# Kernel optimization log

Measured on AMD Instinct MI355X. Metric: run time of the kernel, lower is better.

## Reference

```python
import jax, jax.numpy as jnp
import numpy as np

TEXT_VOCAB = 32000
NUM_CODEBOOKS = 8
CODEBOOK_SIZE = 1024
SLICE = CODEBOOK_SIZE + 2  # codebook slice length incl. BOS/EOS
AUDIO_VOCAB = NUM_CODEBOOKS * SLICE  # 8208
HIDDEN = 2048
NH = 16
NKV = 8
HD = HIDDEN // NH  # 128
FFN = 8192
LAYERS = 2
EPS = 1e-5


def setup_inputs() -> dict:
    key = jax.random.key(0)
    ks = jax.random.split(key, 16)
    s = 0.02
    qkv_dim = (NH + 2 * NKV) * HD  # 4096
    inp = {
        "input_ids": jax.random.randint(ks[0], (2, 1024), 0, TEXT_VOCAB + CODEBOOK_SIZE, dtype=jnp.int32),
        "vocab_embed": jax.random.normal(ks[1], (TEXT_VOCAB, HIDDEN), jnp.float32) * s,
        "audio_embed": jax.random.normal(ks[2], (AUDIO_VOCAB, HIDDEN), jnp.float32) * s,
        "ln_in": jnp.ones((LAYERS, HIDDEN), jnp.float32),
        "ln_audio_in": jnp.ones((LAYERS, HIDDEN), jnp.float32),
        "ln_post": jnp.ones((LAYERS, HIDDEN), jnp.float32),
        "ln_audio_post": jnp.ones((LAYERS, HIDDEN), jnp.float32),
        "w_qkv": jax.random.normal(ks[3], (LAYERS, HIDDEN, qkv_dim), jnp.float32) * s,
        "w_o": jax.random.normal(ks[4], (LAYERS, NH * HD, HIDDEN), jnp.float32) * s,
        "w_fc": jax.random.normal(ks[5], (LAYERS, HIDDEN, FFN), jnp.float32) * s,
        "w_proj": jax.random.normal(ks[6], (LAYERS, FFN, HIDDEN), jnp.float32) * s,
        "w_audio_fc": jax.random.normal(ks[7], (LAYERS, HIDDEN, FFN), jnp.float32) * s,
        "w_audio_proj": jax.random.normal(ks[8], (LAYERS, FFN, HIDDEN), jnp.float32) * s,
        "ln_f": jnp.ones((HIDDEN,), jnp.float32),
    }
    return inp


def _rms(x, w):
    return x * jax.lax.rsqrt(jnp.mean(x * x, axis=-1, keepdims=True) + EPS) * w


def reference(input_ids, vocab_embed, audio_embed, ln_in, ln_audio_in, ln_post,
              ln_audio_post, w_qkv, w_o, w_fc, w_proj, w_audio_fc, w_audio_proj, ln_f):
    B, S = input_ids.shape
    audio_mask = input_ids > TEXT_VOCAB - 1  # [B,S] bool
    mask3 = audio_mask[..., None]

    # --- embedding ---
    text_ids = jnp.where(audio_mask, TEXT_VOCAB - 1, input_ids)
    text_e = vocab_embed[text_ids]  # [B,S,H]
    audio_ids = jnp.where(audio_mask, input_ids - TEXT_VOCAB, 0)
    shift = jnp.arange(NUM_CODEBOOKS, dtype=jnp.int32) * SLICE  # [C]
    audio_e = audio_embed[audio_ids[None] + shift[:, None, None]].sum(0)  # [B,S,H]
    h = jnp.where(mask3, audio_e, text_e)

    causal = jnp.tril(jnp.ones((S, S), bool))
    scale = 1.0 / np.sqrt(HD)

    def layer(h, p):
        li, lai, lp, lap, wqkv, wo, wfc, wpr, wafc, wapr = p
        # dual-path input norm (both computed, merged by mask)
        x = jnp.where(mask3, _rms(h, lai), _rms(h, li))
        # causal GQA attention
        qkv = x @ wqkv
        q = qkv[..., : NH * HD].reshape(B, S, NH, HD)
        k = qkv[..., NH * HD:(NH + NKV) * HD].reshape(B, S, NKV, HD)
        v = qkv[..., (NH + NKV) * HD:].reshape(B, S, NKV, HD)
        rep = NH // NKV
        k = jnp.repeat(k, rep, axis=2)
        v = jnp.repeat(v, rep, axis=2)
        scores = jnp.einsum('bqhd,bkhd->bhqk', q, k) * scale
        scores = jnp.where(causal, scores, jnp.finfo(scores.dtype).min)
        attn = jax.nn.softmax(scores, axis=-1)
        o = jnp.einsum('bhqk,bkhd->bqhd', attn, v).reshape(B, S, NH * HD) @ wo
        h = h + o
        # dual-path FFN (both computed, merged by mask)
        y_text = jax.nn.silu(_rms(h, lp) @ wfc) @ wpr
        y_audio = jax.nn.silu(_rms(h, lap) @ wafc) @ wapr
        h = h + jnp.where(mask3, y_audio, y_text)
        return h, None

    params = (ln_in, ln_audio_in, ln_post, ln_audio_post,
              w_qkv, w_o, w_fc, w_proj, w_audio_fc, w_audio_proj)
    h, _ = jax.lax.scan(layer, h, params)
    return _rms(h, ln_f)
```

## Files before the change

kernel.cpp:

```cpp
#include <hip/hip_runtime.h>
#include <hip/hip_bf16.h>

typedef unsigned short u16;
typedef __attribute__((ext_vector_type(4))) float f32x4;
typedef __attribute__((ext_vector_type(8))) short bf16x8;
typedef __attribute__((ext_vector_type(8))) unsigned short u16x8;
typedef __attribute__((ext_vector_type(4))) unsigned short u16x4;

#define BM 128
#define BN 128
#define BK 64

__device__ __forceinline__ u16 f2bf(float f) {
  union { float f; unsigned u; } v; v.f = f;
  unsigned r = v.u + 0x7FFFu + ((v.u >> 16) & 1u);
  return (u16)(r >> 16);
}
__device__ __forceinline__ float bf2f(u16 v) {
  union { float f; unsigned u; } x; x.u = (unsigned)v << 16; return x.f;
}

__device__ __forceinline__ int xswz(int wg, int n) {
  return (wg & 7) * (n >> 3) + (wg >> 3);
}

__device__ __forceinline__ void g8_stage_half(
    const u16* __restrict__ G, int ldg, int tile, int half, u16* ldsbase) {
  const int tid = threadIdx.x;
#pragma unroll
  for (int load = 0; load < 2; ++load) {
    int unit = load * 512 + tid;
    int row = unit >> 3;
    int seg = (unit & 7) ^ ((unit >> 3) & 7);
    __builtin_amdgcn_global_load_lds(
        (const __attribute__((address_space(1))) void*)(G + (size_t)(half * 128 + row) * ldg + tile * 64 + seg * 8),
        (__attribute__((address_space(3))) void*)(ldsbase + half * 8192 + load * 4096 + (tid >> 6) * 512),
        16, 0, 0);
  }
}

__device__ __forceinline__ void g8_core(
    const u16* __restrict__ A, int lda, const u16* __restrict__ Bt, int ldb,
    int NT, u16* lds, f32x4 acc[8][4]) {
  const int tid = threadIdx.x;
  const int lane = tid & 63;
  const int wid = tid >> 6;
  const int wr = wid >> 2, wc = wid & 3;
  const int lr = lane & 15;
  const int lk4 = lane >> 4;
  const int sw = lane & 7;
  const int off0 = ((lk4 ^ sw) * 8);
  const int off1 = (((4 + lk4) ^ sw) * 8);

  u16* ldsA = lds;
  u16* ldsB = lds + 32768;

  g8_stage_half(A, lda, 0, 0, ldsA);
  g8_stage_half(A, lda, 0, 1, ldsA);
  g8_stage_half(Bt, ldb, 0, 0, ldsB);
  g8_stage_half(Bt, ldb, 0, 1, ldsB);
  if (NT > 1) {
    g8_stage_half(Bt, ldb, 1, 0, ldsB + 16384);
    g8_stage_half(Bt, ldb, 1, 1, ldsB + 16384);
  }
  asm volatile("s_waitcnt vmcnt(4)" ::: "memory");
  __builtin_amdgcn_s_barrier();
  __builtin_amdgcn_sched_barrier(0);

  for (int g = 0; g < NT; ++g) {
    const int buf = g & 1;
    const u16* cA = ldsA + buf * 16384 + wr * 8192;
    const u16* cB = ldsB + buf * 16384;
    bf16x8 bv[4][2];
#pragma unroll
    for (int p = 0; p < 4; ++p) {
      bf16x8 av[2][2];
      if (p == 0) {
#pragma unroll
        for (int n = 0; n < 4; ++n) {
          int rg = wc * 64 + n * 16 + lr;
          const u16* rbase = &cB[(rg >> 7) * 8192 + (rg & 127) * 64];
          bv[n][0] = *(const bf16x8*)&rbase[off0];
          bv[n][1] = *(const bf16x8*)&rbase[off1];
        }
      }
#pragma unroll
      for (int m2 = 0; m2 < 2; ++m2) {
        const u16* rbase = &cA[((p * 2 + m2) * 16 + lr) * 64];
        av[m2][0] = *(const bf16x8*)&rbase[off0];
        av[m2][1] = *(const bf16x8*)&rbase[off1];
      }

      if (p == 0 && g + 1 < NT) g8_stage_half(A, lda, g + 1, 0, ldsA + ((g + 1) & 1) * 16384);
      if (p == 1 && g + 1 < NT) g8_stage_half(A, lda, g + 1, 1, ldsA + ((g + 1) & 1) * 16384);
      if (p == 2 && g + 2 < NT) g8_stage_half(Bt, ldb, g + 2, 0, ldsB + buf * 16384);
      if (p == 3) {
        if (g + 2 < NT) {
          g8_stage_half(Bt, ldb, g + 2, 1, ldsB + buf * 16384);
          asm volatile("s_waitcnt vmcnt(4)" ::: "memory");
        } else if (g + 1 < NT) {
          asm volatile("s_waitcnt vmcnt(0)" ::: "memory");
        }
      }
      __builtin_amdgcn_s_barrier();
      asm volatile("s_waitcnt lgkmcnt(0)" ::: "memory");
      __builtin_amdgcn_sched_barrier(0);
      __builtin_amdgcn_s_setprio(1);
#pragma unroll
      for (int m2 = 0; m2 < 2; ++m2)
#pragma unroll
        for (int n = 0; n < 4; ++n)
#pragma unroll
          for (int kk = 0; kk < 2; ++kk)
            acc[p * 2 + m2][n] = __builtin_amdgcn_mfma_f32_16x16x32_bf16(
                av[m2][kk], bv[n][kk], acc[p * 2 + m2][n], 0, 0, 0);
      __builtin_amdgcn_s_setprio(0);
      __builtin_amdgcn_sched_barrier(0);
      __builtin_amdgcn_s_barrier();
    }
  }
}

__device__ __forceinline__ void g8_acc_zero(f32x4 acc[8][4]) {
#pragma unroll
  for (int m = 0; m < 8; ++m)
#pragma unroll
    for (int n = 0; n < 4; ++n)
      acc[m][n] = (f32x4){0.f, 0.f, 0.f, 0.f};
}

__global__ __launch_bounds__(512, 2) void k_gemm8_qkv(
    const u16* __restrict__ A, const u16* __restrict__ Bt, u16* __restrict__ Pq) {
  __shared__ u16 lds[65536];
  const int wg = xswz(blockIdx.x, 256);
  const int ks = wg >> 7, rem = wg & 127;
  const int tm = rem >> 4, tn = rem & 15;
  f32x4 acc[8][4];
  g8_acc_zero(acc);
  g8_core(A + (size_t)tm * 256 * 2048 + ks * 1024, 2048,
          Bt + (size_t)tn * 256 * 2048 + ks * 1024, 2048, 16, lds, acc);
  const int lane = threadIdx.x & 63, wid = threadIdx.x >> 6;
  const int wr = wid >> 2, wc = wid & 3;
  const int col = lane & 15, rb = (lane >> 4) * 4;
#pragma unroll
  for (int m = 0; m < 8; ++m)
#pragma unroll
    for (int n = 0; n < 4; ++n)
#pragma unroll
      for (int j = 0; j < 4; ++j) {
        int gm = tm * 256 + wr * 128 + m * 16 + rb + j;
        int gn = tn * 256 + wc * 64 + n * 16 + col;
        Pq[((size_t)ks * 2048 + gm) * 4096 + gn] = f2bf(acc[m][n][j]);
      }
}

__global__ __launch_bounds__(512, 2) void k_gemm8_fc(
    const u16* __restrict__ A, const u16* __restrict__ Bt, u16* __restrict__ Cb) {
  __shared__ u16 lds[65536];
  const int wg = xswz(blockIdx.x, 256);
  const int tm = wg >> 5, tn = wg & 31;
  f32x4 acc[8][4];
  g8_acc_zero(acc);
  g8_core(A + (size_t)tm * 256 * 2048, 2048, Bt + (size_t)tn * 256 * 2048, 2048, 32, lds, acc);
  const int lane = threadIdx.x & 63, wid = threadIdx.x >> 6;
  const int wr = wid >> 2, wc = wid & 3;
  const int col = lane & 15, rb = (lane >> 4) * 4;
#pragma unroll
  for (int m = 0; m < 8; ++m)
#pragma unroll
    for (int n = 0; n < 4; ++n)
#pragma unroll
      for (int j = 0; j < 4; ++j) {
        int gm = tm * 256 + wr * 128 + m * 16 + rb + j;
        int gn = tn * 256 + wc * 64 + n * 16 + col;
        float v = acc[m][n][j];
        Cb[(size_t)gm * 8192 + gn] = f2bf(v / (1.f + __expf(-v)));
      }
}

__global__ __launch_bounds__(512, 2) void k_gemm8_sk(
    const u16* __restrict__ A, int lda, const u16* __restrict__ Bt, int ldb,
    int NT, int koff, u16* __restrict__ Pp) {
  __shared__ u16 lds[65536];
  const int wg = xswz(blockIdx.x, 256);
  const int ks = wg >> 6, rem = wg & 63;
  const int tm = rem >> 3, tn = rem & 7;
  f32x4 acc[8][4];
  g8_acc_zero(acc);
  g8_core(A + (size_t)tm * 256 * lda + ks * koff, lda,
          Bt + (size_t)tn * 256 * ldb + ks * koff, ldb, NT, lds, acc);
  const int lane = threadIdx.x & 63, wid = threadIdx.x >> 6;
  const int wr = wid >> 2, wc = wid & 3;
  const int col = lane & 15, rb = (lane >> 4) * 4;
#pragma unroll
  for (int m = 0; m < 8; ++m)
#pragma unroll
    for (int n = 0; n < 4; ++n)
#pragma unroll
      for (int j = 0; j < 4; ++j) {
        int gm = tm * 256 + wr * 128 + m * 16 + rb + j;
        int gn = tn * 256 + wc * 64 + n * 16 + col;
        Pp[((size_t)ks * 2048 + gm) * 2048 + gn] = f2bf(acc[m][n][j]);
      }
}

__global__ __launch_bounds__(256) void k_red_qkv(
    const u16* __restrict__ Pq, u16* __restrict__ Q, u16* __restrict__ Kb,
    u16* __restrict__ VT) {
  const int gm = blockIdx.y;
  const int c = blockIdx.x * 1024 + threadIdx.x * 4;
  const size_t i = (size_t)gm * 4096 + c;
  u16x4 a = *(const u16x4*)&Pq[i];
  u16x4 b2 = *(const u16x4*)&Pq[(size_t)2048 * 4096 + i];
  const int b = gm >> 10, s = gm & 1023;
  u16 v[4];
#pragma unroll
  for (int j = 0; j < 4; ++j) v[j] = f2bf(bf2f(a[j]) + bf2f(b2[j]));
  const int d = c & 127;
  if (c < 2048) {
    int hh = c >> 7;
    *(u16x4*)&Q[((size_t)((b * 16 + hh) * 1024 + s)) * 128 + d] = *(u16x4*)v;
  } else if (c < 3072) {
    int kv = (c - 2048) >> 7;
    *(u16x4*)&Kb[((size_t)((b * 8 + kv) * 1024 + s)) * 128 + d] = *(u16x4*)v;
  } else {
    int kv = (c - 3072) >> 7;
#pragma unroll
    for (int j = 0; j < 4; ++j)
      VT[((size_t)((b * 8 + kv) * 128 + d + j)) * 1024 + s] = v[j];
  }
}

__device__ __forceinline__ void fa_stage128(const u16* __restrict__ G, int ldg, u16* dst,
                                            int nloads) {
  const int tid = threadIdx.x;
  for (int ld = 0; ld < nloads; ++ld) {
    int unit = ld * 256 + tid;
    int row = unit >> 4;
    int seg = (unit & 15) ^ (row & 7);
    __builtin_amdgcn_global_load_lds(
        (const __attribute__((address_space(1))) void*)(G + (size_t)row * ldg + seg * 8),
        (__attribute__((address_space(3))) void*)(dst + ld * 2048 + (tid >> 6) * 512),
        16, 0, 0);
  }
}
__device__ __forceinline__ void fa_stage64(const u16* __restrict__ G, int ldg, u16* dst,
                                           int nloads) {
  const int tid = threadIdx.x;
  for (int ld = 0; ld < nloads; ++ld) {
    int unit = ld * 256 + tid;
    int row = unit >> 3;
    int seg = (unit & 7) ^ (row & 7);
    __builtin_amdgcn_global_load_lds(
        (const __attribute__((address_space(1))) void*)(G + (size_t)row * ldg + seg * 8),
        (__attribute__((address_space(3))) void*)(dst + ld * 2048 + (tid >> 6) * 512),
        16, 0, 0);
  }
}

__global__ __launch_bounds__(256, 2) void k_fattn(
    const u16* __restrict__ Q, const u16* __restrict__ Kb, const u16* __restrict__ VT,
    u16* __restrict__ O) {
  const int tm = blockIdx.x;
  const int bh = blockIdx.y;
  const int b = bh >> 4, hq = bh & 15, kv = hq >> 1;
  __shared__ u16 lds[32768];
  u16* Klds = lds;
  u16* Vlds = lds + 8192;
  u16* Plds = lds + 24576;
  const int lane = threadIdx.x & 63, wave = threadIdx.x >> 6;
  const int wm = wave * 32;
  const int lr = lane & 15, lk = lane >> 4;
  const int rb = lk * 4;
  const int cl = lr;

  const u16* Qg = Q + ((size_t)(b * 16 + hq) * 1024 + tm * 128) * 128;
  fa_stage128(Qg, 128, lds, 8);
  asm volatile("s_waitcnt vmcnt(0)" ::: "memory");
  __builtin_amdgcn_s_barrier();
  __builtin_amdgcn_sched_barrier(0);
  bf16x8 qf[2][4];
#pragma unroll
  for (int m = 0; m < 2; ++m)
#pragma unroll
    for (int kk = 0; kk < 4; ++kk) {
      int row = wm + m * 16 + lr;
      qf[m][kk] = *(const bf16x8*)&lds[row * 128 + (((kk * 4 + lk) ^ (lr & 7)) * 8)];
    }
  asm volatile("s_waitcnt lgkmcnt(0)" ::: "memory");
  __builtin_amdgcn_s_barrier();
  __builtin_amdgcn_sched_barrier(0);

  const u16* Kg = Kb + (size_t)(b * 8 + kv) * 1024 * 128;
  const u16* Vg = VT + (size_t)(b * 8 + kv) * 128 * 1024;
  const int NT = 2 * (tm + 1);
  fa_stage128(Kg, 128, Klds, 4);
  fa_stage64(Vg, 1024, Vlds, 4);

  f32x4 accO[2][8];
#pragma unroll
  for (int m = 0; m < 2; ++m)
#pragma unroll
    for (int n = 0; n < 8; ++n) accO[m][n] = (f32x4){0.f, 0.f, 0.f, 0.f};
  float mst[8], lst[8];
#pragma unroll
  for (int i = 0; i < 8; ++i) { mst[i] = -3.0e38f; lst[i] = 0.f; }
  const float scale = 0.08838834764831845f;

  for (int t = 0; t < NT; ++t) {
    asm volatile("s_waitcnt vmcnt(0)" ::: "memory");
    __builtin_amdgcn_s_barrier();
    __builtin_amdgcn_sched_barrier(0);
    u16* Vcur = Vlds + (t & 1) * 8192;
    f32x4 accS[2][4];
#pragma unroll
    for (int m = 0; m < 2; ++m)
#pragma unroll
      for (int n = 0; n < 4; ++n) accS[m][n] = (f32x4){0.f, 0.f, 0.f, 0.f};
#pragma unroll
    for (int kk = 0; kk < 4; ++kk) {
      bf16x8 kf[4];
#pragma unroll
      for (int n = 0; n < 4; ++n)
        kf[n] = *(const bf16x8*)&Klds[(n * 16 + lr) * 128 + (((kk * 4 + lk) ^ (lr & 7)) * 8)];
#pragma unroll
      for (int m = 0; m < 2; ++m)
#pragma unroll
        for (int n = 0; n < 4; ++n)
          accS[m][n] = __builtin_amdgcn_mfma_f32_16x16x32_bf16(qf[m][kk], kf[n], accS[m][n], 0, 0, 0);
    }
    asm volatile("s_waitcnt lgkmcnt(0)" ::: "memory");
    __builtin_amdgcn_s_barrier();
    __builtin_amdgcn_sched_barrier(0);
    if (t + 1 < NT) {
      fa_stage128(Kg + (size_t)(t + 1) * 64 * 128, 128, Klds, 4);
      fa_stage64(Vg + (t + 1) * 64, 1024, Vlds + ((t + 1) & 1) * 8192, 4);
    }
    const bool dm = (t >= 2 * tm);
#pragma unroll
    for (int m = 0; m < 2; ++m)
#pragma unroll
      for (int j = 0; j < 4; ++j) {
        const int si = m * 4 + j;
        const int rglob = tm * 128 + wm + m * 16 + rb + j;
        float v[4];
        float vmax = -3.0e38f;
#pragma unroll
        for (int n = 0; n < 4; ++n) {
          float x = accS[m][n][j] * scale;
          if (dm && (t * 64 + n * 16 + cl > rglob)) x = -3.0e38f;
          v[n] = x;
          vmax = fmaxf(vmax, x);
        }
#pragma unroll
        for (int o = 1; o < 16; o <<= 1) vmax = fmaxf(vmax, __shfl_xor(vmax, o));
        float mnew = fmaxf(mst[si], vmax);
        float alpha = __expf(mst[si] - mnew);
        mst[si] = mnew;
        float rs = 0.f;
        const int prow = wm + m * 16 + rb + j;
#pragma unroll
        for (int n = 0; n < 4; ++n) {
          float pp = __expf(v[n] - mnew);
          rs += pp;
          int col = n * 16 + cl;
          Plds[prow * 64 + (((col >> 3) ^ (prow & 7)) * 8) + (col & 7)] = f2bf(pp);
        }
#pragma unroll
        for (int o = 1; o < 16; o <<= 1) rs += __shfl_xor(rs, o);
        lst[si] = lst[si] * alpha + rs;
#pragma unroll
        for (int n = 0; n < 8; ++n) accO[m][n][j] *= alpha;
      }
#pragma unroll
    for (int kk = 0; kk < 2; ++kk) {
      bf16x8 pf[2], vf[8];
#pragma unroll
      for (int m = 0; m < 2; ++m) {
        int prow = wm + m * 16 + lr;
        pf[m] = *(const bf16x8*)&Plds[prow * 64 + (((kk * 4 + lk) ^ (lr & 7)) * 8)];
      }
#pragma unroll
      for (int n = 0; n < 8; ++n) {
        int d = n * 16 + lr;
        vf[n] = *(const bf16x8*)&Vcur[d * 64 + (((kk * 4 + lk) ^ (d & 7)) * 8)];
      }
#pragma unroll
      for (int m = 0; m < 2; ++m)
#pragma unroll
        for (int n = 0; n < 8; ++n)
          accO[m][n] = __builtin_amdgcn_mfma_f32_16x16x32_bf16(pf[m], vf[n], accO[m][n], 0, 0, 0);
    }
  }
#pragma unroll
  for (int m = 0; m < 2; ++m)
#pragma unroll
    for (int j = 0; j < 4; ++j) {
      float invl = 1.f / lst[m * 4 + j];
      int s = tm * 128 + wm + m * 16 + rb + j;
#pragma unroll
      for (int n = 0; n < 8; ++n) {
        int d = n * 16 + cl;
        O[(size_t)(b * 1024 + s) * 2048 + hq * 128 + d] = f2bf(accO[m][n][j] * invl);
      }
    }
}

__device__ __forceinline__ void acc_zero(f32x4 acc[4][4]) {
#pragma unroll
  for (int m = 0; m < 4; ++m)
#pragma unroll
    for (int n = 0; n < 4; ++n)
      acc[m][n] = (f32x4){0.f, 0.f, 0.f, 0.f};
}

__device__ __forceinline__ void gemm_core_db(
    const u16* __restrict__ A, int lda,
    const u16* __restrict__ Bt, int ldb,
    int ksteps, int amax, u16* sA, u16* sB, f32x4 acc[4][4]) {
  const int tid = threadIdx.x;
  const int wave = tid >> 6;
  const int lane = tid & 63;
  const int r = tid >> 3;
  const int ksw = (tid & 7) ^ ((tid >> 3) & 7);
  const int wm = (wave >> 1) * 64;
  const int wn = (wave & 1) * 64;
  const int lr = lane & 15;
  const int lk4 = lane >> 4;
  const int sw = lane & 7;
  const int off0 = ((lk4 ^ sw) * 8);
  const int off1 = (((4 + lk4) ^ sw) * 8);

  auto stage = [&](int buf, int kt) {
    const int k0 = kt * BK;
    u16* dA = sA + buf * 8192 + wave * 512;
    u16* dB = sB + buf * 8192 + wave * 512;
#pragma unroll
    for (int i = 0; i < 4; ++i) {
      int ra = i * 32 + r; if (ra > amax) ra = amax;
      __builtin_amdgcn_global_load_lds(
          (const __attribute__((address_space(1))) void*)(A + (size_t)ra * lda + k0 + ksw * 8),
          (__attribute__((address_space(3))) void*)(dA + i * 2048), 16, 0, 0);
      __builtin_amdgcn_global_load_lds(
          (const __attribute__((address_space(1))) void*)(Bt + (size_t)(i * 32 + r) * ldb + k0 + ksw * 8),
          (__attribute__((address_space(3))) void*)(dB + i * 2048), 16, 0, 0);
    }
  };

  stage(0, 0);
  asm volatile("s_waitcnt vmcnt(0)" ::: "memory");
  __builtin_amdgcn_s_barrier();
  __builtin_amdgcn_sched_barrier(0);

  for (int kt = 0; kt < ksteps; ++kt) {
    const int cur = kt & 1;
    if (kt + 1 < ksteps) stage(cur ^ 1, kt + 1);
    const u16* cA = sA + cur * 8192;
    const u16* cB = sB + cur * 8192;
#pragma unroll
    for (int kk = 0; kk < 2; ++kk) {
      const int off = kk ? off1 : off0;
      bf16x8 av[4], bv[4];
#pragma unroll
      for (int m = 0; m < 4; ++m)
        av[m] = *(const bf16x8*)&cA[(wm + m * 16 + lr) * BK + off];
#pragma unroll
      for (int n = 0; n < 4; ++n)
        bv[n] = *(const bf16x8*)&cB[(wn + n * 16 + lr) * BK + off];
#pragma unroll
      for (int m = 0; m < 4; ++m)
#pragma unroll
        for (int n = 0; n < 4; ++n)
          acc[m][n] = __builtin_amdgcn_mfma_f32_16x16x32_bf16(av[m], bv[n], acc[m][n], 0, 0, 0);
    }
    asm volatile("s_waitcnt vmcnt(0)" ::: "memory");
    __builtin_amdgcn_s_barrier();
    __builtin_amdgcn_sched_barrier(0);
  }
}

__global__ __launch_bounds__(256) void k_gemm_cs(
    const u16* __restrict__ A, int lda, const u16* __restrict__ Bt, int ldb,
    int ksteps, int ntn, u16* __restrict__ Pp, const int* __restrict__ cnt) {
  const int Na = cnt[0];
  const int tm = blockIdx.y;
  if (tm * 128 >= Na) return;
  const int tn = blockIdx.x % ntn;
  const int ks = blockIdx.x / ntn;
  const int ldc = ntn * 128;
  const int k0 = ks * ksteps * BK;
  __shared__ u16 sA[2 * BM * BK], sB[2 * BN * BK];
  f32x4 acc[4][4];
  acc_zero(acc);
  gemm_core_db(A + (size_t)tm * 128 * lda + k0, lda, Bt + (size_t)tn * 128 * ldb + k0, ldb,
               ksteps, Na - 1 - tm * 128, sA, sB, acc);
  const int lane = threadIdx.x & 63, wave = threadIdx.x >> 6;
  const int wm = (wave >> 1) * 64, wn = (wave & 1) * 64;
  const int col = lane & 15, rb = (lane >> 4) * 4;
#pragma unroll
  for (int m = 0; m < 4; ++m)
#pragma unroll
    for (int n = 0; n < 4; ++n)
#pragma unroll
      for (int j = 0; j < 4; ++j) {
        int gm = tm * 128 + wm + m * 16 + rb + j;
        int gn = tn * 128 + wn + n * 16 + col;
        Pp[((size_t)ks * 256 + gm) * ldc + gn] = f2bf(acc[m][n][j]);
      }
}

__global__ __launch_bounds__(256) void k_red4_silu(
    const u16* __restrict__ Pp, u16* __restrict__ t1, const int* __restrict__ cnt) {
  const int row = blockIdx.y;
  if (row >= cnt[0]) return;
  const int c = blockIdx.x * 1024 + threadIdx.x * 4;
  const size_t i = (size_t)row * 8192 + c;
  float s[4] = {0.f, 0.f, 0.f, 0.f};
#pragma unroll
  for (int k = 0; k < 4; ++k) {
    u16x4 a = *(const u16x4*)&Pp[(size_t)k * 256 * 8192 + i];
#pragma unroll
    for (int j = 0; j < 4; ++j) s[j] += bf2f(a[j]);
  }
  u16x4 ov;
#pragma unroll
  for (int j = 0; j < 4; ++j) {
    float v = s[j];
    ov[j] = f2bf(v / (1.f + __expf(-v)));
  }
  *(u16x4*)&t1[i] = ov;
}

__global__ __launch_bounds__(256) void k_transpose_all(
    const float* __restrict__ w_qkv, const float* __restrict__ w_o,
    const float* __restrict__ w_fc, const float* __restrict__ w_proj,
    const float* __restrict__ w_afc, const float* __restrict__ w_aproj,
    u16* __restrict__ WtAll) {
  int bid = blockIdx.x;
  int l = 0;
  if (bid >= 19456) { l = 1; bid -= 19456; }
  const float* src;
  u16* dst;
  int K, N, t;
  u16* WtL = WtAll + (size_t)l * 79691776;
  if (bid < 2048)       { src = w_qkv  + (size_t)l * 8388608;  dst = WtL;            K = 2048; N = 4096; t = bid; }
  else if (bid < 3072)  { src = w_o    + (size_t)l * 4194304;  dst = WtL + 8388608;  K = 2048; N = 2048; t = bid - 2048; }
  else if (bid < 7168)  { src = w_fc   + (size_t)l * 16777216; dst = WtL + 12582912; K = 2048; N = 8192; t = bid - 3072; }
  else if (bid < 11264) { src = w_proj + (size_t)l * 16777216; dst = WtL + 29360128; K = 8192; N = 2048; t = bid - 7168; }
  else if (bid < 15360) { src = w_afc  + (size_t)l * 16777216; dst = WtL + 46137344; K = 2048; N = 8192; t = bid - 11264; }
  else                  { src = w_aproj+ (size_t)l * 16777216; dst = WtL + 62914560; K = 8192; N = 2048; t = bid - 15360; }
  const int nk = K >> 6;
  const int sb = t >> 6, w = t & 63;
  const int nsbk = nk >> 3;
  const int tk = ((sb % nsbk) << 3) + (w & 7);
  const int tn = ((sb / nsbk) << 3) + (w >> 3);
  const int tid = threadIdx.x;
  __shared__ float tile[64][65];
#pragma unroll
  for (int i = 0; i < 4; ++i) {
    int idx = i * 256 + tid;
    int r = idx >> 4, c4 = (idx & 15) * 4;
    float4 v = *(const float4*)&src[(size_t)(tk * 64 + r) * N + tn * 64 + c4];
    tile[r][c4]     = v.x;
    tile[r][c4 + 1] = v.y;
    tile[r][c4 + 2] = v.z;
    tile[r][c4 + 3] = v.w;
  }
  __syncthreads();
#pragma unroll
  for (int i = 0; i < 2; ++i) {
    int u = i * 256 + tid;
    int n = u >> 3, seg = u & 7;
    u16x8 ov;
#pragma unroll
    for (int j = 0; j < 8; ++j) ov[j] = f2bf(tile[seg * 8 + j][n]);
    *(u16x8*)&dst[(size_t)(tn * 64 + n) * K + tk * 64 + seg * 8] = ov;
  }
}

__global__ __launch_bounds__(256) void k_scan(
    const int* __restrict__ mask, int* __restrict__ cpos,
    int* __restrict__ cidx, int* __restrict__ cnt) {
  const int tid = threadIdx.x;
  const int lane = tid & 63, wid = tid >> 6;
  int m[8];
  int s = 0;
#pragma unroll
  for (int j = 0; j < 8; ++j) { m[j] = mask[tid * 8 + j]; s += m[j]; }
  int ps = s;
#pragma unroll
  for (int o = 1; o < 64; o <<= 1) {
    int t = __shfl_up(ps, o);
    if (lane >= o) ps += t;
  }
  __shared__ int wsum[4];
  if (lane == 63) wsum[wid] = ps;
  __syncthreads();
  int base = 0;
  for (int w = 0; w < wid; ++w) base += wsum[w];
  int run = base + ps - s;
#pragma unroll
  for (int j = 0; j < 8; ++j) {
    int row = tid * 8 + j;
    cpos[row] = run;
    if (m[j]) cidx[run] = row;
    run += m[j];
  }
  if (tid == 255) cnt[0] = run;
}

__device__ __forceinline__ float block_sum256(float v, float* red) {
  const int tid = threadIdx.x;
#pragma unroll
  for (int o = 32; o; o >>= 1) v += __shfl_xor(v, o);
  if ((tid & 63) == 0) red[tid >> 6] = v;
  __syncthreads();
  float r = red[0] + red[1] + red[2] + red[3];
  __syncthreads();
  return r;
}

__global__ __launch_bounds__(256) void k_embed_rms(
    const int* __restrict__ ids, const float* __restrict__ vocab,
    const float* __restrict__ audio, const float* __restrict__ wt,
    const float* __restrict__ wa, float* __restrict__ h, int* __restrict__ mask,
    u16* __restrict__ x) {
  const int t = blockIdx.x;
  const int tid = threadIdx.x;
  const int id = ids[t];
  const int am = (id > 31999) ? 1 : 0;
  if (tid == 0) mask[t] = am;
  float* hr = h + (size_t)t * 2048;
  const int c0 = tid * 8;
  float4 v0, v1;
  if (!am) {
    const float4* src = (const float4*)(vocab + (size_t)id * 2048);
    v0 = src[tid * 2];
    v1 = src[tid * 2 + 1];
  } else {
    const int aid = id - 32000;
    v0 = (float4){0.f, 0.f, 0.f, 0.f};
    v1 = (float4){0.f, 0.f, 0.f, 0.f};
#pragma unroll
    for (int c = 0; c < 8; ++c) {
      const float4* ap = (const float4*)(audio + (size_t)(aid + c * 1026) * 2048);
      float4 a0 = ap[tid * 2], a1 = ap[tid * 2 + 1];
      v0.x += a0.x; v0.y += a0.y; v0.z += a0.z; v0.w += a0.w;
      v1.x += a1.x; v1.y += a1.y; v1.z += a1.z; v1.w += a1.w;
    }
  }
  ((float4*)hr)[tid * 2] = v0;
  ((float4*)hr)[tid * 2 + 1] = v1;
  const float* f0 = (const float*)&v0;
  const float* f1 = (const float*)&v1;
  float ss = 0.f;
#pragma unroll
  for (int j = 0; j < 4; ++j) ss += f0[j] * f0[j] + f1[j] * f1[j];
  __shared__ float red[4];
  ss = block_sum256(ss, red);
  const float inv = rsqrtf(ss * (1.0f / 2048.0f) + 1e-5f);
  const float* w = am ? wa : wt;
  u16x8 a;
#pragma unroll
  for (int j = 0; j < 8; ++j) {
    float hv = (j < 4 ? f0[j] : f1[j - 4]) * inv;
    a[j] = f2bf(hv * w[c0 + j]);
  }
  *(u16x8*)&x[(size_t)t * 2048 + c0] = a;
}

__global__ __launch_bounds__(256) void k_redrms_post(
    float* __restrict__ h, const u16* __restrict__ Pp,
    const float* __restrict__ wt, const float* __restrict__ wa,
    const int* __restrict__ mask, u16* __restrict__ x, u16* __restrict__ xc,
    const int* __restrict__ cpos) {
  const int row = blockIdx.x, tid = threadIdx.x;
  const int c0 = tid * 8;
  const size_t base = (size_t)row * 2048 + c0;
  float4 a0 = *(const float4*)&h[base];
  float4 a1 = *(const float4*)&h[base + 4];
  float* fa0 = (float*)&a0;
  float* fa1 = (float*)&a1;
#pragma unroll
  for (int k = 0; k < 4; ++k) {
    u16x8 pv = *(const u16x8*)&Pp[(size_t)k * 2048 * 2048 + base];
#pragma unroll
    for (int j = 0; j < 4; ++j) fa0[j] += bf2f(pv[j]);
#pragma unroll
    for (int j = 0; j < 4; ++j) fa1[j] += bf2f(pv[4 + j]);
  }
  *(float4*)&h[base] = a0;
  *(float4*)&h[base + 4] = a1;
  float ss = 0.f;
#pragma unroll
  for (int j = 0; j < 4; ++j) ss += fa0[j] * fa0[j] + fa1[j] * fa1[j];
  __shared__ float red[4];
  ss = block_sum256(ss, red);
  const float inv = rsqrtf(ss * (1.0f / 2048.0f) + 1e-5f);
  u16x8 xv;
#pragma unroll
  for (int j = 0; j < 8; ++j) {
    float hv = (j < 4 ? fa0[j] : fa1[j - 4]) * inv;
    xv[j] = f2bf(hv * wt[c0 + j]);
  }
  *(u16x8*)&x[base] = xv;
  if (mask[row]) {
    u16x8 av;
#pragma unroll
    for (int j = 0; j < 8; ++j) {
      float hv = (j < 4 ? fa0[j] : fa1[j - 4]) * inv;
      av[j] = f2bf(hv * wa[c0 + j]);
    }
    *(u16x8*)&xc[(size_t)cpos[row] * 2048 + c0] = av;
  }
}

__global__ __launch_bounds__(256) void k_redrms_ffn(
    float* __restrict__ h, const u16* __restrict__ Psk, const u16* __restrict__ Pap,
    const float* __restrict__ wt, const float* __restrict__ wa,
    const float* __restrict__ wf, const int* __restrict__ mask,
    const int* __restrict__ cpos, u16* __restrict__ x, float* __restrict__ outf, int fin) {
  const int row = blockIdx.x, tid = threadIdx.x;
  const int c0 = tid * 8;
  const size_t base = (size_t)row * 2048 + c0;
  float4 a0 = *(const float4*)&h[base];
  float4 a1 = *(const float4*)&h[base + 4];
  float* fa0 = (float*)&a0;
  float* fa1 = (float*)&a1;
  if (mask[row] == 0) {
#pragma unroll
    for (int k = 0; k < 4; ++k) {
      u16x8 pv = *(const u16x8*)&Psk[(size_t)k * 2048 * 2048 + base];
#pragma unroll
      for (int j = 0; j < 4; ++j) fa0[j] += bf2f(pv[j]);
#pragma unroll
      for (int j = 0; j < 4; ++j) fa1[j] += bf2f(pv[4 + j]);
    }
  } else {
    const size_t cb = (size_t)cpos[row] * 2048 + c0;
#pragma unroll
    for (int k = 0; k < 8; ++k) {
      u16x8 pv = *(const u16x8*)&Pap[(size_t)k * 256 * 2048 + cb];
#pragma unroll
      for (int j = 0; j < 4; ++j) fa0[j] += bf2f(pv[j]);
#pragma unroll
      for (int j = 0; j < 4; ++j) fa1[j] += bf2f(pv[4 + j]);
    }
  }
  if (!fin) {
    *(float4*)&h[base] = a0;
    *(float4*)&h[base + 4] = a1;
  }
  float ss = 0.f;
#pragma unroll
  for (int j = 0; j < 4; ++j) ss += fa0[j] * fa0[j] + fa1[j] * fa1[j];
  __shared__ float red[4];
  ss = block_sum256(ss, red);
  const float inv = rsqrtf(ss * (1.0f / 2048.0f) + 1e-5f);
  if (fin) {
    float4 o0, o1;
    float* p0 = (float*)&o0;
    float* p1 = (float*)&o1;
#pragma unroll
    for (int j = 0; j < 4; ++j) {
      p0[j] = fa0[j] * inv * wf[c0 + j];
      p1[j] = fa1[j] * inv * wf[c0 + 4 + j];
    }
    *(float4*)&outf[base] = o0;
    *(float4*)&outf[base + 4] = o1;
  } else {
    const float* w = mask[row] ? wa : wt;
    u16x8 xv;
#pragma unroll
    for (int j = 0; j < 8; ++j) {
      float hv = (j < 4 ? fa0[j] : fa1[j - 4]) * inv;
      xv[j] = f2bf(hv * w[c0 + j]);
    }
    *(u16x8*)&x[base] = xv;
  }
}

extern "C" void kernel_launch(void* const* d_in, const int* in_sizes, int n_in,
                              void* d_out, int out_size, void* d_ws, size_t ws_size,
                              hipStream_t stream) {
  const int* ids = (const int*)d_in[0];
  const float* vocab = (const float*)d_in[1];
  const float* audio = (const float*)d_in[2];
  const float* ln_in = (const float*)d_in[3];
  const float* ln_audio_in = (const float*)d_in[4];
  const float* ln_post = (const float*)d_in[5];
  const float* ln_audio_post = (const float*)d_in[6];
  const float* w_qkv = (const float*)d_in[7];
  const float* w_o = (const float*)d_in[8];
  const float* w_fc = (const float*)d_in[9];
  const float* w_proj = (const float*)d_in[10];
  const float* w_afc = (const float*)d_in[11];
  const float* w_aproj = (const float*)d_in[12];
  const float* ln_f = (const float*)d_in[13];
  float* out = (float*)d_out;

  char* p = (char*)d_ws;
  auto alloc = [&](size_t bytes) {
    char* r = p;
    p += (bytes + 255) & ~(size_t)255;
    return r;
  };
  float* h   = (float*)alloc((size_t)2048 * 2048 * 4);
  u16* x     = (u16*)alloc((size_t)2048 * 2048 * 2);
  u16* xc    = (u16*)alloc((size_t)2048 * 2048 * 2);
  u16* o     = (u16*)alloc((size_t)2048 * 2048 * 2);
  int* mask  = (int*)alloc((size_t)2048 * 4);
  int* cpos  = (int*)alloc((size_t)2048 * 4);
  int* cidx  = (int*)alloc((size_t)2048 * 4);
  int* cnt   = (int*)alloc((size_t)64 * 4);
  u16* WtAll = (u16*)alloc((size_t)2 * 79691776 * 2);
  u16* Q     = (u16*)alloc((size_t)2 * 16 * 1024 * 128 * 2);
  u16* Kb    = (u16*)alloc((size_t)2 * 8 * 1024 * 128 * 2);
  u16* VT    = (u16*)alloc((size_t)2 * 8 * 1024 * 128 * 2);
  char* A    = alloc((size_t)96 * 1024 * 1024);
  char* Bg   = alloc((size_t)16 * 1024 * 1024);
  u16* t1    = (u16*)alloc((size_t)2048 * 8192 * 2);
  u16* Pq    = (u16*)A;
  u16* Psk   = (u16*)A;
  u16* Pafc  = (u16*)(A + (size_t)67108864);
  u16* Paprj = (u16*)Bg;
  (void)ws_size; (void)in_sizes; (void)n_in; (void)out_size;

  k_transpose_all<<<38912, 256, 0, stream>>>(w_qkv, w_o, w_fc, w_proj, w_afc, w_aproj, WtAll);
  k_embed_rms<<<2048, 256, 0, stream>>>(ids, vocab, audio, ln_in, ln_audio_in, h, mask, x);
  k_scan<<<1, 256, 0, stream>>>(mask, cpos, cidx, cnt);

  for (int l = 0; l < 2; ++l) {
    u16* WtL = WtAll + (size_t)l * 79691776;
    u16* Wqkv_t  = WtL;
    u16* Wo_t    = WtL + 8388608;
    u16* Wfc_t   = WtL + 12582912;
    u16* Wproj_t = WtL + 29360128;
    u16* Wafc_t  = WtL + 46137344;
    u16* Waprj_t = WtL + 62914560;

    k_gemm8_qkv<<<256, 512, 0, stream>>>(x, Wqkv_t, Pq);
    k_red_qkv<<<dim3(4, 2048), 256, 0, stream>>>(Pq, Q, Kb, VT);
    k_fattn<<<dim3(8, 32), 256, 0, stream>>>(Q, Kb, VT, o);
    k_gemm8_sk<<<256, 512, 0, stream>>>(o, 2048, Wo_t, 2048, 8, 512, Psk);
    k_redrms_post<<<2048, 256, 0, stream>>>(h, Psk, ln_post + l * 2048,
                                            ln_audio_post + l * 2048, mask, x, xc, cpos);
    k_gemm8_fc<<<256, 512, 0, stream>>>(x, Wfc_t, t1);
    k_gemm8_sk<<<256, 512, 0, stream>>>(t1, 8192, Wproj_t, 8192, 32, 2048, Psk);
    k_gemm_cs<<<dim3(64 * 4, 2), 256, 0, stream>>>(xc, 2048, Wafc_t, 2048, 8, 64, Pafc, cnt);
    k_red4_silu<<<dim3(8, 256), 256, 0, stream>>>(Pafc, t1, cnt);
    k_gemm_cs<<<dim3(16 * 8, 2), 256, 0, stream>>>(t1, 8192, Waprj_t, 8192, 16, 16, Paprj, cnt);
    if (l == 0)
      k_redrms_ffn<<<2048, 256, 0, stream>>>(h, Psk, Paprj, ln_in + 2048,
                                             ln_audio_in + 2048, nullptr, mask, cpos, x,
                                             nullptr, 0);
    else
      k_redrms_ffn<<<2048, 256, 0, stream>>>(h, Psk, Paprj, nullptr, nullptr, ln_f, mask,
                                             cpos, nullptr, out, 1);
  }
}
```

Baseline: 959.0 us.

## Read fp32 audio FFN weights directly in compacted GEMM, drop their pre-transpose

The audio FFN weights are no longer transposed and converted to bf16 in the upfront transpose kernel. The compacted-row GEMM now loads the fp32 weights straight from global memory into registers, converts them to bf16 and writes them swizzled into LDS inside the main loop. This removes a large read/write pass over the audio weights that served only a few audio rows. The cost is heavier per-tile B loads (fp32, register staged), which may slow the GEMM itself.

```diff
diff --git a/kernel.cpp b/kernel.cpp
--- a/kernel.cpp
+++ b/kernel.cpp
@@ -414,73 +414,8 @@
       acc[m][n] = (f32x4){0.f, 0.f, 0.f, 0.f};
 }
 
-__device__ __forceinline__ void gemm_core_db(
-    const u16* __restrict__ A, int lda,
-    const u16* __restrict__ Bt, int ldb,
-    int ksteps, int amax, u16* sA, u16* sB, f32x4 acc[4][4]) {
-  const int tid = threadIdx.x;
-  const int wave = tid >> 6;
-  const int lane = tid & 63;
-  const int r = tid >> 3;
-  const int ksw = (tid & 7) ^ ((tid >> 3) & 7);
-  const int wm = (wave >> 1) * 64;
-  const int wn = (wave & 1) * 64;
-  const int lr = lane & 15;
-  const int lk4 = lane >> 4;
-  const int sw = lane & 7;
-  const int off0 = ((lk4 ^ sw) * 8);
-  const int off1 = (((4 + lk4) ^ sw) * 8);
-
-  auto stage = [&](int buf, int kt) {
-    const int k0 = kt * BK;
-    u16* dA = sA + buf * 8192 + wave * 512;
-    u16* dB = sB + buf * 8192 + wave * 512;
-#pragma unroll
-    for (int i = 0; i < 4; ++i) {
-      int ra = i * 32 + r; if (ra > amax) ra = amax;
-      __builtin_amdgcn_global_load_lds(
-          (const __attribute__((address_space(1))) void*)(A + (size_t)ra * lda + k0 + ksw * 8),
-          (__attribute__((address_space(3))) void*)(dA + i * 2048), 16, 0, 0);
-      __builtin_amdgcn_global_load_lds(
-          (const __attribute__((address_space(1))) void*)(Bt + (size_t)(i * 32 + r) * ldb + k0 + ksw * 8),
-          (__attribute__((address_space(3))) void*)(dB + i * 2048), 16, 0, 0);
-    }
-  };
-
-  stage(0, 0);
-  asm volatile("s_waitcnt vmcnt(0)" ::: "memory");
-  __builtin_amdgcn_s_barrier();
-  __builtin_amdgcn_sched_barrier(0);
-
-  for (int kt = 0; kt < ksteps; ++kt) {
-    const int cur = kt & 1;
-    if (kt + 1 < ksteps) stage(cur ^ 1, kt + 1);
-    const u16* cA = sA + cur * 8192;
-    const u16* cB = sB + cur * 8192;
-#pragma unroll
-    for (int kk = 0; kk < 2; ++kk) {
-      const int off = kk ? off1 : off0;
-      bf16x8 av[4], bv[4];
-#pragma unroll
-      for (int m = 0; m < 4; ++m)
-        av[m] = *(const bf16x8*)&cA[(wm + m * 16 + lr) * BK + off];
-#pragma unroll
-      for (int n = 0; n < 4; ++n)
-        bv[n] = *(const bf16x8*)&cB[(wn + n * 16 + lr) * BK + off];
-#pragma unroll
-      for (int m = 0; m < 4; ++m)
-#pragma unroll
-        for (int n = 0; n < 4; ++n)
-          acc[m][n] = __builtin_amdgcn_mfma_f32_16x16x32_bf16(av[m], bv[n], acc[m][n], 0, 0, 0);
-    }
-    asm volatile("s_waitcnt vmcnt(0)" ::: "memory");
-    __builtin_amdgcn_s_barrier();
-    __builtin_amdgcn_sched_barrier(0);
-  }
-}
-
-__global__ __launch_bounds__(256) void k_gemm_cs(
-    const u16* __restrict__ A, int lda, const u16* __restrict__ Bt, int ldb,
+__global__ __launch_bounds__(256) void k_gemm_csf(
+    const u16* __restrict__ A, int lda, const float* __restrict__ Wf, int ldw,
     int ksteps, int ntn, u16* __restrict__ Pp, const int* __restrict__ cnt) {
   const int Na = cnt[0];
   const int tm = blockIdx.y;
@@ -492,10 +427,91 @@
   __shared__ u16 sA[2 * BM * BK], sB[2 * BN * BK];
   f32x4 acc[4][4];
   acc_zero(acc);
-  gemm_core_db(A + (size_t)tm * 128 * lda + k0, lda, Bt + (size_t)tn * 128 * ldb + k0, ldb,
-               ksteps, Na - 1 - tm * 128, sA, sB, acc);
-  const int lane = threadIdx.x & 63, wave = threadIdx.x >> 6;
+
+  const u16* Ab = A + (size_t)tm * 128 * lda + k0;
+  const float* Wb = Wf + (size_t)k0 * ldw + tn * 128;
+
+  const int tid = threadIdx.x;
+  const int wave = tid >> 6, lane = tid & 63;
+  const int r = tid >> 3;
+  const int ksw = (tid & 7) ^ ((tid >> 3) & 7);
   const int wm = (wave >> 1) * 64, wn = (wave & 1) * 64;
+  const int lr = lane & 15, lk4 = lane >> 4, sw = lane & 7;
+  const int off0 = ((lk4 ^ sw) * 8), off1 = (((4 + lk4) ^ sw) * 8);
+  const int amax = Na - 1 - tm * 128;
+  const int bk_ = tid >> 5;
+  const int bn4 = (tid & 31) * 4;
+
+  float4 breg[8];
+
+  auto stageA = [&](int buf, int kt) {
+    u16* dA = sA + buf * 8192 + wave * 512;
+    const int kk0 = kt * BK;
+#pragma unroll
+    for (int i = 0; i < 4; ++i) {
+      int ra = i * 32 + r; if (ra > amax) ra = amax;
+      __builtin_amdgcn_global_load_lds(
+          (const __attribute__((address_space(1))) void*)(Ab + (size_t)ra * lda + kk0 + ksw * 8),
+          (__attribute__((address_space(3))) void*)(dA + i * 2048), 16, 0, 0);
+    }
+  };
+  auto loadB = [&](int kt) {
+#pragma unroll
+    for (int i = 0; i < 8; ++i) {
+      int kk_ = kt * 64 + i * 8 + bk_;
+      breg[i] = *(const float4*)&Wb[(size_t)kk_ * ldw + bn4];
+    }
+  };
+  auto writeB = [&](int buf) {
+    u16* dB = sB + buf * 8192;
+#pragma unroll
+    for (int i = 0; i < 8; ++i) {
+      int kk_ = i * 8 + bk_;
+      const float* bf = (const float*)&breg[i];
+#pragma unroll
+      for (int j = 0; j < 4; ++j) {
+        int n = bn4 + j;
+        dB[n * 64 + (((kk_ >> 3) ^ (n & 7)) * 8) + (kk_ & 7)] = f2bf(bf[j]);
+      }
+    }
+  };
+
+  stageA(0, 0);
+  loadB(0);
+  asm volatile("s_waitcnt vmcnt(0)" ::: "memory");
+  writeB(0);
+  asm volatile("s_waitcnt lgkmcnt(0)" ::: "memory");
+  __builtin_amdgcn_s_barrier();
+  __builtin_amdgcn_sched_barrier(0);
+
+  for (int kt = 0; kt < ksteps; ++kt) {
+    const int cur = kt & 1;
+    if (kt + 1 < ksteps) { stageA(cur ^ 1, kt + 1); loadB(kt + 1); }
+    const u16* cA = sA + cur * 8192;
+    const u16* cB = sB + cur * 8192;
+#pragma unroll
+    for (int kk = 0; kk < 2; ++kk) {
+      const int off = kk ? off1 : off0;
+      bf16x8 av[4], bv[4];
+#pragma unroll
+      for (int m = 0; m < 4; ++m)
+        av[m] = *(const bf16x8*)&cA[(wm + m * 16 + lr) * BK + off];
+#pragma unroll
+      for (int n = 0; n < 4; ++n)
+        bv[n] = *(const bf16x8*)&cB[(wn + n * 16 + lr) * BK + off];
+#pragma unroll
+      for (int m = 0; m < 4; ++m)
+#pragma unroll
+        for (int n = 0; n < 4; ++n)
+          acc[m][n] = __builtin_amdgcn_mfma_f32_16x16x32_bf16(av[m], bv[n], acc[m][n], 0, 0, 0);
+    }
+    asm volatile("s_waitcnt vmcnt(0)" ::: "memory");
+    if (kt + 1 < ksteps) writeB(cur ^ 1);
+    asm volatile("s_waitcnt lgkmcnt(0)" ::: "memory");
+    __builtin_amdgcn_s_barrier();
+    __builtin_amdgcn_sched_barrier(0);
+  }
+
   const int col = lane & 15, rb = (lane >> 4) * 4;
 #pragma unroll
   for (int m = 0; m < 4; ++m)
@@ -534,21 +550,18 @@
 __global__ __launch_bounds__(256) void k_transpose_all(
     const float* __restrict__ w_qkv, const float* __restrict__ w_o,
     const float* __restrict__ w_fc, const float* __restrict__ w_proj,
-    const float* __restrict__ w_afc, const float* __restrict__ w_aproj,
     u16* __restrict__ WtAll) {
   int bid = blockIdx.x;
   int l = 0;
-  if (bid >= 19456) { l = 1; bid -= 19456; }
+  if (bid >= 11264) { l = 1; bid -= 11264; }
   const float* src;
   u16* dst;
   int K, N, t;
-  u16* WtL = WtAll + (size_t)l * 79691776;
+  u16* WtL = WtAll + (size_t)l * 46137344;
   if (bid < 2048)       { src = w_qkv  + (size_t)l * 8388608;  dst = WtL;            K = 2048; N = 4096; t = bid; }
   else if (bid < 3072)  { src = w_o    + (size_t)l * 4194304;  dst = WtL + 8388608;  K = 2048; N = 2048; t = bid - 2048; }
   else if (bid < 7168)  { src = w_fc   + (size_t)l * 16777216; dst = WtL + 12582912; K = 2048; N = 8192; t = bid - 3072; }
-  else if (bid < 11264) { src = w_proj + (size_t)l * 16777216; dst = WtL + 29360128; K = 8192; N = 2048; t = bid - 7168; }
-  else if (bid < 15360) { src = w_afc  + (size_t)l * 16777216; dst = WtL + 46137344; K = 2048; N = 8192; t = bid - 11264; }
-  else                  { src = w_aproj+ (size_t)l * 16777216; dst = WtL + 62914560; K = 8192; N = 2048; t = bid - 15360; }
+  else                  { src = w_proj + (size_t)l * 16777216; dst = WtL + 29360128; K = 8192; N = 2048; t = bid - 7168; }
   const int nk = K >> 6;
   const int sb = t >> 6, w = t & 63;
   const int nsbk = nk >> 3;
@@ -813,7 +826,7 @@
   int* cpos  = (int*)alloc((size_t)2048 * 4);
   int* cidx  = (int*)alloc((size_t)2048 * 4);
   int* cnt   = (int*)alloc((size_t)64 * 4);
-  u16* WtAll = (u16*)alloc((size_t)2 * 79691776 * 2);
+  u16* WtAll = (u16*)alloc((size_t)2 * 46137344 * 2);
   u16* Q     = (u16*)alloc((size_t)2 * 16 * 1024 * 128 * 2);
   u16* Kb    = (u16*)alloc((size_t)2 * 8 * 1024 * 128 * 2);
   u16* VT    = (u16*)alloc((size_t)2 * 8 * 1024 * 128 * 2);
@@ -826,18 +839,16 @@
   u16* Paprj = (u16*)Bg;
   (void)ws_size; (void)in_sizes; (void)n_in; (void)out_size;
 
-  k_transpose_all<<<38912, 256, 0, stream>>>(w_qkv, w_o, w_fc, w_proj, w_afc, w_aproj, WtAll);
+  k_transpose_all<<<22528, 256, 0, stream>>>(w_qkv, w_o, w_fc, w_proj, WtAll);
   k_embed_rms<<<2048, 256, 0, stream>>>(ids, vocab, audio, ln_in, ln_audio_in, h, mask, x);
   k_scan<<<1, 256, 0, stream>>>(mask, cpos, cidx, cnt);
 
   for (int l = 0; l < 2; ++l) {
-    u16* WtL = WtAll + (size_t)l * 79691776;
+    u16* WtL = WtAll + (size_t)l * 46137344;
     u16* Wqkv_t  = WtL;
     u16* Wo_t    = WtL + 8388608;
     u16* Wfc_t   = WtL + 12582912;
     u16* Wproj_t = WtL + 29360128;
-    u16* Wafc_t  = WtL + 46137344;
-    u16* Waprj_t = WtL + 62914560;
 
     k_gemm8_qkv<<<256, 512, 0, stream>>>(x, Wqkv_t, Pq);
     k_red_qkv<<<dim3(4, 2048), 256, 0, stream>>>(Pq, Q, Kb, VT);
@@ -847,9 +858,11 @@
                                             ln_audio_post + l * 2048, mask, x, xc, cpos);
     k_gemm8_fc<<<256, 512, 0, stream>>>(x, Wfc_t, t1);
     k_gemm8_sk<<<256, 512, 0, stream>>>(t1, 8192, Wproj_t, 8192, 32, 2048, Psk);
-    k_gemm_cs<<<dim3(64 * 4, 2), 256, 0, stream>>>(xc, 2048, Wafc_t, 2048, 8, 64, Pafc, cnt);
+    k_gemm_csf<<<dim3(64 * 4, 2), 256, 0, stream>>>(
+        xc, 2048, w_afc + (size_t)l * 2048 * 8192, 8192, 8, 64, Pafc, cnt);
     k_red4_silu<<<dim3(8, 256), 256, 0, stream>>>(Pafc, t1, cnt);
-    k_gemm_cs<<<dim3(16 * 8, 2), 256, 0, stream>>>(t1, 8192, Waprj_t, 8192, 16, 16, Paprj, cnt);
+    k_gemm_csf<<<dim3(16 * 8, 2), 256, 0, stream>>>(
+        t1, 8192, w_aproj + (size_t)l * 8192 * 2048, 2048, 16, 16, Paprj, cnt);
     if (l == 0)
       k_redrms_ffn<<<2048, 256, 0, stream>>>(h, Psk, Paprj, ln_in + 2048,
                                              ln_audio_in + 2048, nullptr, mask, cpos, x,
```

New measurement: 971.2 us. About the same (+1.3%).
